# Kernel optimization log

Hardware: AMD Instinct MI355X
Metric: run time of the kernel (lower is better)

## Reference

```python
import jax, jax.numpy as jnp
import numpy as np

N = 100000
E = 1_600_000
IN_CH = 64
HID = 32       # per-head hidden dim
HEADS = 4
OUT_CH = 6
NEG_SLOPE = 0.2


def _glorot(key, shape):
    fan_in, fan_out = shape[0], shape[-1]
    lim = jnp.sqrt(6.0 / (fan_in + fan_out))
    return jax.random.uniform(key, shape, jnp.float32, -lim, lim)


def setup_inputs() -> dict:
    key = jax.random.key(0)
    ks = jax.random.split(key, 20)
    x = jax.random.normal(ks[0], (N, IN_CH), jnp.float32)
    edge_index = jax.random.randint(ks[1], (2, E), 0, N, jnp.int64)
    batch = jnp.zeros((N,), jnp.int64)
    inp = {"x": x, "edge_index": edge_index, "batch": batch}
    inp["W0"] = _glorot(ks[2], (IN_CH, HEADS * HID))
    inp["as0"] = _glorot(ks[3], (HEADS, HID))
    inp["ad0"] = _glorot(ks[4], (HEADS, HID))
    inp["b0"] = jnp.zeros((HEADS * HID,), jnp.float32)
    inp["W1"] = _glorot(ks[5], (HEADS * HID, HEADS * HID))
    inp["as1"] = _glorot(ks[6], (HEADS, HID))
    inp["ad1"] = _glorot(ks[7], (HEADS, HID))
    inp["b1"] = jnp.zeros((HEADS * HID,), jnp.float32)
    inp["W2"] = _glorot(ks[8], (HEADS * HID, HEADS * HID))
    inp["as2"] = _glorot(ks[9], (HEADS, HID))
    inp["ad2"] = _glorot(ks[10], (HEADS, HID))
    inp["b2"] = jnp.zeros((HEADS * HID,), jnp.float32)
    # final layer: 128 -> 6, 1 head, no concat (mean)
    inp["W3"] = _glorot(ks[11], (HEADS * HID, OUT_CH))
    inp["as3"] = _glorot(ks[12], (1, OUT_CH))
    inp["ad3"] = _glorot(ks[13], (1, OUT_CH))
    inp["b3"] = jnp.zeros((OUT_CH,), jnp.float32)
    return inp


def gat_conv(x, src, dst, W, a_src, a_dst, b, heads, concat):
    """PyG GATConv: linear -> per-edge attention -> segment softmax over dst -> scatter-add."""
    n = x.shape[0]
    h = (x @ W).reshape(n, heads, -1)                       # [N,H,D]
    al_s = jnp.sum(h * a_src, axis=-1)                      # [N,H]
    al_d = jnp.sum(h * a_dst, axis=-1)                      # [N,H]
    e = jax.nn.leaky_relu(al_s[src] + al_d[dst], NEG_SLOPE)  # [E,H]
    m = jax.ops.segment_max(e, dst, num_segments=n)         # segment softmax (stable)
    ex = jnp.exp(e - m[dst])
    s = jax.ops.segment_sum(ex, dst, num_segments=n)
    alpha = ex / (s[dst] + 1e-16)                           # [E,H]
    out = jax.ops.segment_sum(alpha[:, :, None] * h[src], dst, num_segments=n)  # [N,H,D]
    out = out.reshape(n, -1) if concat else out.mean(axis=1)
    return out + b


def reference(x, edge_index, batch, W0, as0, ad0, b0, W1, as1, ad1, b1,
              W2, as2, ad2, b2, W3, as3, ad3, b3):
    n = x.shape[0]
    # PyG GATConv adds self-loops by default; edge set is static (no pooling), add once.
    ar = jnp.arange(n, dtype=edge_index.dtype)
    ei = jnp.concatenate([edge_index, jnp.stack([ar, ar])], axis=1)
    src, dst = ei[0], ei[1]
    x = jax.nn.elu(gat_conv(x, src, dst, W0, as0, ad0, b0, HEADS, True))
    x = jax.nn.elu(gat_conv(x, src, dst, W1, as1, ad1, b1, HEADS, True))
    x = jax.nn.elu(gat_conv(x, src, dst, W2, as2, ad2, b2, HEADS, True))
    x = gat_conv(x, src, dst, W3, as3, ad3, b3, 1, False)   # final layer: no activation
    return x
```

## Files before the change

kernel.cpp:

```cpp
#include <hip/hip_runtime.h>
#include <hip/hip_bf16.h>
#include <hip/hip_fp16.h>

#define IN_CH 64
#define HID 32
#define HEADS 4
#define OUT_CH 6
#define NEG_SLOPE 0.2f

typedef __attribute__((ext_vector_type(8))) _Float16 half8;
typedef __attribute__((ext_vector_type(4))) float f32x4;


#define PBLK 256
#define CAP 6144

__global__ __launch_bounds__(256) void part_count(const int* __restrict__ ei, int E, int EN,
                                                  int NB, int epb, int* __restrict__ counts) {
    __shared__ int cnt[512];
    int b = blockIdx.x, t = threadIdx.x;
    for (int i = t; i < NB; i += 256) cnt[i] = 0;
    __syncthreads();
    int e0 = b * epb;
    int e1 = min(e0 + epb, EN);
    for (int e = e0 + t; e < e1; e += 256) {
        int d = (e < E) ? ei[E + e] : (e - E);
        atomicAdd(&cnt[d >> 8], 1);
    }
    __syncthreads();
    for (int i = t; i < NB; i += 256) counts[(size_t)i * PBLK + b] = cnt[i];
}

__global__ __launch_bounds__(256) void bucket_tot(const int* __restrict__ counts,
                                                  int* __restrict__ btot) {
    __shared__ int red[256];
    int k = blockIdx.x, t = threadIdx.x;
    red[t] = counts[(size_t)k * PBLK + t];
    __syncthreads();
    for (int off = 128; off; off >>= 1) {
        if (t < off) red[t] += red[t + off];
        __syncthreads();
    }
    if (t == 0) btot[k] = red[0];
}

__global__ __launch_bounds__(256) void bucket_scan(const int* __restrict__ btot, int NB, int EN,
                                                   int* __restrict__ bstart) {
    __shared__ int tmp[256];
    int t = threadIdx.x;
    int chunk = (NB + 255) >> 8;
    int s0 = t * chunk, s1 = min(s0 + chunk, NB);
    int sum = 0;
    for (int i = s0; i < s1; ++i) sum += btot[i];
    tmp[t] = sum;
    __syncthreads();
    for (int off = 1; off < 256; off <<= 1) {
        int v = (t >= off) ? tmp[t - off] : 0;
        __syncthreads();
        tmp[t] += v;
        __syncthreads();
    }
    int run = (t == 0) ? 0 : tmp[t - 1];
    for (int i = s0; i < s1; ++i) {
        int c = btot[i];
        bstart[i] = run;
        run += c;
    }
    if (t == 255) bstart[NB] = EN;
}

__global__ __launch_bounds__(256) void bucket_base(int* __restrict__ counts,
                                                   const int* __restrict__ bstart) {
    __shared__ int sc[256];
    int k = blockIdx.x, t = threadIdx.x;
    int v = counts[(size_t)k * PBLK + t];
    sc[t] = v;
    __syncthreads();
    for (int off = 1; off < 256; off <<= 1) {
        int u = (t >= off) ? sc[t - off] : 0;
        __syncthreads();
        sc[t] += u;
        __syncthreads();
    }
    counts[(size_t)k * PBLK + t] = bstart[k] + sc[t] - v;
}

__global__ __launch_bounds__(256) void part_scatter(const int* __restrict__ ei, int E, int EN,
                                                    int NB, int epb,
                                                    const int* __restrict__ base,
                                                    int2* __restrict__ ebuf) {
    __shared__ int cur[512];
    int b = blockIdx.x, t = threadIdx.x;
    for (int i = t; i < NB; i += 256) cur[i] = base[(size_t)i * PBLK + b];
    __syncthreads();
    int e0 = b * epb;
    int e1 = min(e0 + epb, EN);
    for (int e = e0 + t; e < e1; e += 256) {
        int s, d;
        if (e < E) { s = ei[e]; d = ei[E + e]; }
        else       { s = e - E; d = s; }
        int slot = atomicAdd(&cur[d >> 8], 1);
        ebuf[slot] = make_int2(s, d & 255);
    }
}

__global__ __launch_bounds__(256) void bucket_csr(const int2* __restrict__ ebuf,
                                                  const int* __restrict__ bstart,
                                                  int NB, int N, int EN,
                                                  int* __restrict__ row_start,
                                                  int* __restrict__ csr_src) {
    __shared__ int cnt[256];
    __shared__ int sc[256];
    __shared__ int stage[CAP];
    int k = blockIdx.x, t = threadIdx.x;
    int s0 = bstart[k], s1 = bstart[k + 1];
    int len = s1 - s0;
    cnt[t] = 0;
    __syncthreads();
    for (int i = t; i < len; i += 256) atomicAdd(&cnt[ebuf[s0 + i].y], 1);
    __syncthreads();
    int v = cnt[t];
    sc[t] = v;
    __syncthreads();
    for (int off = 1; off < 256; off <<= 1) {
        int u = (t >= off) ? sc[t - off] : 0;
        __syncthreads();
        sc[t] += u;
        __syncthreads();
    }
    int excl = sc[t] - v;
    int g = (k << 8) + t;
    if (g < N) row_start[g] = s0 + excl;
    if (k == NB - 1 && t == 0) row_start[N] = EN;
    bool fits = (len <= CAP);
    cnt[t] = fits ? excl : s0 + excl;
    __syncthreads();
    if (fits) {
        for (int i = t; i < len; i += 256) {
            int2 e = ebuf[s0 + i];
            int slot = atomicAdd(&cnt[e.y], 1);
            stage[slot] = e.x;
        }
        __syncthreads();
        for (int i = t; i < len; i += 256) csr_src[s0 + i] = stage[i];
    } else {
        for (int i = t; i < len; i += 256) {
            int2 e = ebuf[s0 + i];
            int slot = atomicAdd(&cnt[e.y], 1);
            csr_src[slot] = e.x;
        }
    }
}


__global__ void wtrans_all(const float* __restrict__ W0, const float* __restrict__ W1,
                           const float* __restrict__ W2, __half* __restrict__ WT0,
                           __half* __restrict__ WT1, __half* __restrict__ WT2) {
    int o = blockIdx.x * blockDim.x + threadIdx.x;
    if (o < 8192) {
        int c = o >> 6, k = o & 63;
        WT0[o] = __float2half(W0[(size_t)k * 128 + c]);
    } else if (o < 8192 + 16384) {
        int i = o - 8192;
        int c = i >> 7, k = i & 127;
        WT1[i] = __float2half(W1[(size_t)k * 128 + c]);
    } else if (o < 8192 + 32768) {
        int i = o - 8192 - 16384;
        int c = i >> 7, k = i & 127;
        WT2[i] = __float2half(W2[(size_t)k * 128 + c]);
    }
}


__global__ __launch_bounds__(256) void gemm_mfma(const __half* __restrict__ A,
                                                 const float* __restrict__ Af,
                                                 const __half* __restrict__ WT,
                                                 const float* __restrict__ avs,
                                                 const float* __restrict__ avd,
                                                 __half* __restrict__ C,
                                                 float* __restrict__ als,
                                                 float* __restrict__ ald,
                                                 int N, int K) {
    int tid = threadIdx.x;
    int wv = tid >> 6, lane = tid & 63;
    int row0 = blockIdx.x * 64 + wv * 16;
    int lrow = lane & 15;
    int lk = (lane >> 4) * 8;
    int garow = row0 + lrow;

    half8 afrag[4];
#pragma unroll
    for (int ks = 0; ks < 4; ++ks) {
        half8 z = {(_Float16)0, (_Float16)0, (_Float16)0, (_Float16)0,
                   (_Float16)0, (_Float16)0, (_Float16)0, (_Float16)0};
        afrag[ks] = z;
    }
    if (garow < N) {
        if (K == 128) {
            const __half* ap = A + (size_t)garow * 128 + lk;
#pragma unroll
            for (int ks = 0; ks < 4; ++ks)
                afrag[ks] = *reinterpret_cast<const half8*>(ap + ks * 32);
        } else {
            const float* ap = Af + (size_t)garow * 64 + lk;
#pragma unroll
            for (int ks = 0; ks < 2; ++ks) {
                float4 f0 = *reinterpret_cast<const float4*>(ap + ks * 32);
                float4 f1 = *reinterpret_cast<const float4*>(ap + ks * 32 + 4);
                half8 fr = {(_Float16)f0.x, (_Float16)f0.y, (_Float16)f0.z, (_Float16)f0.w,
                            (_Float16)f1.x, (_Float16)f1.y, (_Float16)f1.z, (_Float16)f1.w};
                afrag[ks] = fr;
            }
        }
    }

    f32x4 acc[8];
#pragma unroll
    for (int t = 0; t < 8; ++t) acc[t] = (f32x4){0.f, 0.f, 0.f, 0.f};

#pragma unroll
    for (int t = 0; t < 8; ++t) {
        const __half* wb = WT + (size_t)(t * 16 + lrow) * K + lk;
        if (K == 128) {
#pragma unroll
            for (int ks = 0; ks < 4; ++ks) {
                half8 bfrag = *reinterpret_cast<const half8*>(wb + ks * 32);
                acc[t] = __builtin_amdgcn_mfma_f32_16x16x32_f16(afrag[ks], bfrag, acc[t], 0, 0, 0);
            }
        } else {
#pragma unroll
            for (int ks = 0; ks < 2; ++ks) {
                half8 bfrag = *reinterpret_cast<const half8*>(wb + ks * 32);
                acc[t] = __builtin_amdgcn_mfma_f32_16x16x32_f16(afrag[ks], bfrag, acc[t], 0, 0, 0);
            }
        }
    }

    int rbase = (lane >> 4) * 4;
#pragma unroll
    for (int t = 0; t < 8; ++t) {
#pragma unroll
        for (int j = 0; j < 4; ++j) {
            int gr = row0 + rbase + j;
            if (gr < N) C[(size_t)gr * 128 + t * 16 + lrow] = __float2half(acc[t][j]);
        }
    }
    float ps[4][4], pd[4][4];
#pragma unroll
    for (int h = 0; h < 4; ++h)
#pragma unroll
        for (int j = 0; j < 4; ++j) { ps[h][j] = 0.f; pd[h][j] = 0.f; }
#pragma unroll
    for (int t = 0; t < 8; ++t) {
        int ht = t >> 1;
        float as_c = avs[t * 16 + lrow];
        float ad_c = avd[t * 16 + lrow];
#pragma unroll
        for (int j = 0; j < 4; ++j) {
            ps[ht][j] += acc[t][j] * as_c;
            pd[ht][j] += acc[t][j] * ad_c;
        }
    }
#pragma unroll
    for (int h = 0; h < 4; ++h) {
#pragma unroll
        for (int j = 0; j < 4; ++j) {
            float s = ps[h][j], d = pd[h][j];
            s += __shfl_xor(s, 1); d += __shfl_xor(d, 1);
            s += __shfl_xor(s, 2); d += __shfl_xor(d, 2);
            s += __shfl_xor(s, 4); d += __shfl_xor(d, 4);
            s += __shfl_xor(s, 8); d += __shfl_xor(d, 8);
            if (lrow == 0) {
                int gr = row0 + rbase + j;
                if (gr < N) {
                    als[(size_t)gr * 4 + h] = s;
                    ald[(size_t)gr * 4 + h] = d;
                }
            }
        }
    }
}


__device__ __forceinline__ float lrelu(float x) { return x > 0.f ? x : NEG_SLOPE * x; }

__global__ __launch_bounds__(256) void agg_kernel(const __half* __restrict__ h,
                                                  const float* __restrict__ als4,
                                                  const float* __restrict__ ald4,
                                                  const int* __restrict__ row_start,
                                                  const int* __restrict__ csr_src,
                                                  const float* __restrict__ bias,
                                                  __half* __restrict__ xout,
                                                  int N, int applyElu) {
    int v = (int)((blockIdx.x * blockDim.x + threadIdx.x) >> 6);
    int lane = threadIdx.x & 63;
    if (v >= N) return;
    int base = row_start[v], end = row_start[v + 1];

    int half_ = lane >> 5;
    int dim4 = (lane & 31) * 4;
    int hd2  = (lane & 31) >> 3;

    float aldh = ald4[(size_t)v * 4 + hd2];
    float alsh = als4[(size_t)v * 4 + hd2];
    float em = lrelu(alsh + aldh);

    const char* hB = (const char*)h;
    const char* aB = (const char*)als4;
    unsigned dby = (unsigned)dim4 * 2;
    unsigned aby = (unsigned)hd2 * 4;

    float4 acc  = make_float4(0.f, 0.f, 0.f, 0.f);
    float4 acc2 = make_float4(0.f, 0.f, 0.f, 0.f);
    float ssum = 0.f, ssum2 = 0.f;

    union H4 { uint2 u; __half hh[4]; };

    int j = base + half_;
    for (; j + 6 < end; j += 8) {
        unsigned s0 = (unsigned)csr_src[j + 0];
        unsigned s1 = (unsigned)csr_src[j + 2];
        unsigned s2 = (unsigned)csr_src[j + 4];
        unsigned s3 = (unsigned)csr_src[j + 6];
        float a0 = *(const float*)(aB + (s0 << 4) + aby);
        float a1 = *(const float*)(aB + (s1 << 4) + aby);
        float a2 = *(const float*)(aB + (s2 << 4) + aby);
        float a3 = *(const float*)(aB + (s3 << 4) + aby);
        H4 r0, r1, r2, r3;
        r0.u = *(const uint2*)(hB + (s0 << 8) + dby);
        r1.u = *(const uint2*)(hB + (s1 << 8) + dby);
        r2.u = *(const uint2*)(hB + (s2 << 8) + dby);
        r3.u = *(const uint2*)(hB + (s3 << 8) + dby);
        float e0 = __expf(lrelu(a0 + aldh) - em);
        float e1 = __expf(lrelu(a1 + aldh) - em);
        float e2 = __expf(lrelu(a2 + aldh) - em);
        float e3 = __expf(lrelu(a3 + aldh) - em);
        ssum  += e0 + e2;
        ssum2 += e1 + e3;
        acc.x  += e0 * (float)r0.hh[0]; acc.y  += e0 * (float)r0.hh[1];
        acc.z  += e0 * (float)r0.hh[2]; acc.w  += e0 * (float)r0.hh[3];
        acc2.x += e1 * (float)r1.hh[0]; acc2.y += e1 * (float)r1.hh[1];
        acc2.z += e1 * (float)r1.hh[2]; acc2.w += e1 * (float)r1.hh[3];
        acc.x  += e2 * (float)r2.hh[0]; acc.y  += e2 * (float)r2.hh[1];
        acc.z  += e2 * (float)r2.hh[2]; acc.w  += e2 * (float)r2.hh[3];
        acc2.x += e3 * (float)r3.hh[0]; acc2.y += e3 * (float)r3.hh[1];
        acc2.z += e3 * (float)r3.hh[2]; acc2.w += e3 * (float)r3.hh[3];
    }
    for (; j < end; j += 2) {
        unsigned s0 = (unsigned)csr_src[j];
        float a0 = *(const float*)(aB + (s0 << 4) + aby);
        H4 r0;
        r0.u = *(const uint2*)(hB + (s0 << 8) + dby);
        float e0 = __expf(lrelu(a0 + aldh) - em);
        ssum += e0;
        acc.x += e0 * (float)r0.hh[0]; acc.y += e0 * (float)r0.hh[1];
        acc.z += e0 * (float)r0.hh[2]; acc.w += e0 * (float)r0.hh[3];
    }
    acc.x += acc2.x; acc.y += acc2.y; acc.z += acc2.z; acc.w += acc2.w;
    ssum += ssum2;
    acc.x += __shfl_xor(acc.x, 32);
    acc.y += __shfl_xor(acc.y, 32);
    acc.z += __shfl_xor(acc.z, 32);
    acc.w += __shfl_xor(acc.w, 32);
    ssum  += __shfl_xor(ssum, 32);

    if (lane < 32) {
        float inv = 1.0f / (ssum + 1e-16f);
        float4 bv = *reinterpret_cast<const float4*>(bias + dim4);
        float4 o;
        o.x = acc.x * inv + bv.x;
        o.y = acc.y * inv + bv.y;
        o.z = acc.z * inv + bv.z;
        o.w = acc.w * inv + bv.w;
        if (applyElu) {
            o.x = o.x > 0.f ? o.x : expm1f(o.x);
            o.y = o.y > 0.f ? o.y : expm1f(o.y);
            o.z = o.z > 0.f ? o.z : expm1f(o.z);
            o.w = o.w > 0.f ? o.w : expm1f(o.w);
        }
        __half2* op = reinterpret_cast<__half2*>(xout + (size_t)v * 128 + dim4);
        op[0] = __float22half2_rn(make_float2(o.x, o.y));
        op[1] = __float22half2_rn(make_float2(o.z, o.w));
    }
}


__global__ void gemm3_kernel(const __half* __restrict__ x, const float* __restrict__ W,
                             const float* __restrict__ as3, const float* __restrict__ ad3,
                             float* __restrict__ h3p, float* __restrict__ als3,
                             float* __restrict__ ald3, int N) {
    int n = blockIdx.x * blockDim.x + threadIdx.x;
    if (n >= N) return;
    float acc[6] = {0.f, 0.f, 0.f, 0.f, 0.f, 0.f};
    const __half* xp = x + (size_t)n * 128;
#pragma unroll 2
    for (int k8 = 0; k8 < 16; ++k8) {
        union { uint4 u; __half hh[8]; } rv;
        rv.u = *reinterpret_cast<const uint4*>(xp + k8 * 8);
        const float* w0 = W + (size_t)(k8 * 8) * 6;
#pragma unroll
        for (int kk = 0; kk < 8; ++kk) {
            float xv = (float)rv.hh[kk];
#pragma unroll
            for (int q = 0; q < 6; ++q)
                acc[q] += xv * w0[kk * 6 + q];
        }
    }
    float s = 0.f, d = 0.f;
#pragma unroll
    for (int q = 0; q < 6; ++q) {
        s += acc[q] * as3[q];
        d += acc[q] * ad3[q];
    }
    float4* hp = reinterpret_cast<float4*>(h3p + (size_t)n * 8);
    hp[0] = make_float4(acc[0], acc[1], acc[2], acc[3]);
    hp[1] = make_float4(acc[4], acc[5], 0.f, 0.f);
    als3[n] = s;
    ald3[n] = d;
}


__global__ __launch_bounds__(256) void agg3_kernel(const float* __restrict__ h3p,
                                                   const float* __restrict__ als3,
                                                   const float* __restrict__ ald3,
                                                   const int* __restrict__ row_start,
                                                   const int* __restrict__ csr_src,
                                                   const float* __restrict__ b3,
                                                   float* __restrict__ out, int N) {
    int v = (int)((blockIdx.x * blockDim.x + threadIdx.x) >> 5);
    int lane = threadIdx.x & 31;
    if (v >= N) return;
    int base = row_start[v], end = row_start[v + 1];
    int slot = lane >> 3;
    int dim  = lane & 7;

    float aldv = ald3[v];
    float em = lrelu(als3[v] + aldv);
    float acc = 0.f, ssum = 0.f;
    const char* hB = (const char*)h3p;
    const char* aB = (const char*)als3;
    unsigned dby = (unsigned)dim * 4;

    for (int j = base + slot; j < end; j += 4) {
        unsigned s = (unsigned)csr_src[j];
        float a = *(const float*)(aB + (s << 2));
        float hv = *(const float*)(hB + (s << 5) + dby);
        float e = __expf(lrelu(a + aldv) - em);
        ssum += e;
        acc += e * hv;
    }
    acc  += __shfl_xor(acc, 8);
    acc  += __shfl_xor(acc, 16);
    ssum += __shfl_xor(ssum, 8);
    ssum += __shfl_xor(ssum, 16);

    if (slot == 0 && dim < 6) {
        float inv = 1.f / (ssum + 1e-16f);
        out[(size_t)v * 6 + dim] = acc * inv + b3[dim];
    }
}


extern "C" void kernel_launch(void* const* d_in, const int* in_sizes, int n_in,
                              void* d_out, int out_size, void* d_ws, size_t ws_size,
                              hipStream_t stream) {
    const float* x    = (const float*)d_in[0];
    const int*   ei   = (const int*)d_in[1];
    const float* W0   = (const float*)d_in[3];
    const float* as0  = (const float*)d_in[4];
    const float* ad0  = (const float*)d_in[5];
    const float* b0   = (const float*)d_in[6];
    const float* W1   = (const float*)d_in[7];
    const float* as1  = (const float*)d_in[8];
    const float* ad1  = (const float*)d_in[9];
    const float* b1   = (const float*)d_in[10];
    const float* W2   = (const float*)d_in[11];
    const float* as2  = (const float*)d_in[12];
    const float* ad2  = (const float*)d_in[13];
    const float* b2   = (const float*)d_in[14];
    const float* W3   = (const float*)d_in[15];
    const float* as3  = (const float*)d_in[16];
    const float* ad3  = (const float*)d_in[17];
    const float* b3   = (const float*)d_in[18];
    float* out = (float*)d_out;

    int N = in_sizes[0] / IN_CH;
    int E = in_sizes[1] / 2;
    int EN = E + N;
    int NB = (N + 255) >> 8;
    int epb = (EN + PBLK - 1) / PBLK;

    char* p = (char*)d_ws;
    auto alloc = [&](size_t bytes) {
        char* q = p;
        p += (bytes + 255) & ~(size_t)255;
        return q;
    };
    __half* hbuf = (__half*)alloc((size_t)N * 128 * 2);
    __half* xA   = (__half*)alloc((size_t)N * 128 * 2);
    __half* xB   = (__half*)alloc((size_t)N * 128 * 2);
    __half* WT0  = (__half*)alloc((size_t)128 * 64 * 2);
    __half* WT1  = (__half*)alloc((size_t)128 * 128 * 2);
    __half* WT2  = (__half*)alloc((size_t)128 * 128 * 2);
    float* als  = (float*)alloc((size_t)N * 4 * 4);
    float* ald  = (float*)alloc((size_t)N * 4 * 4);
    float* h3p  = (float*)alloc((size_t)N * 8 * 4);
    float* als3 = (float*)alloc((size_t)N * 4);
    float* ald3 = (float*)alloc((size_t)N * 4);
    int* row_start = (int*)alloc((size_t)(N + 1) * 4);
    int* csr_src   = (int*)alloc((size_t)EN * 4);
    int2* ebuf     = (int2*)alloc((size_t)EN * 8);
    int* counts    = (int*)alloc((size_t)NB * PBLK * 4);
    int* btot      = (int*)alloc((size_t)NB * 4);
    int* bstart    = (int*)alloc((size_t)(NB + 1) * 4);
    (void)ws_size; (void)n_in; (void)out_size;

    part_count<<<PBLK, 256, 0, stream>>>(ei, E, EN, NB, epb, counts);
    bucket_tot<<<NB, 256, 0, stream>>>(counts, btot);
    bucket_scan<<<1, 256, 0, stream>>>(btot, NB, EN, bstart);
    bucket_base<<<NB, 256, 0, stream>>>(counts, bstart);
    part_scatter<<<PBLK, 256, 0, stream>>>(ei, E, EN, NB, epb, counts, ebuf);
    bucket_csr<<<NB, 256, 0, stream>>>(ebuf, bstart, NB, N, EN, row_start, csr_src);

    wtrans_all<<<(8192 + 32768 + 255) / 256, 256, 0, stream>>>(W0, W1, W2, WT0, WT1, WT2);

    int gemm_grid = (N + 63) / 64;
    int agg_grid  = (N + 3) / 4;
    int n_grid    = (N + 255) / 256;
    int agg3_grid = (N + 7) / 8;

    gemm_mfma<<<gemm_grid, 256, 0, stream>>>(nullptr, x, WT0, as0, ad0, hbuf, als, ald, N, 64);
    agg_kernel<<<agg_grid, 256, 0, stream>>>(hbuf, als, ald, row_start, csr_src, b0, xA, N, 1);

    gemm_mfma<<<gemm_grid, 256, 0, stream>>>(xA, nullptr, WT1, as1, ad1, hbuf, als, ald, N, 128);
    agg_kernel<<<agg_grid, 256, 0, stream>>>(hbuf, als, ald, row_start, csr_src, b1, xB, N, 1);

    gemm_mfma<<<gemm_grid, 256, 0, stream>>>(xB, nullptr, WT2, as2, ad2, hbuf, als, ald, N, 128);
    agg_kernel<<<agg_grid, 256, 0, stream>>>(hbuf, als, ald, row_start, csr_src, b2, xA, N, 1);

    gemm3_kernel<<<n_grid, 256, 0, stream>>>(xA, W3, as3, ad3, h3p, als3, ald3, N);
    agg3_kernel<<<agg3_grid, 256, 0, stream>>>(h3p, als3, ald3, row_start, csr_src, b3, out, N);
}
```

Before: 443.3 us.

## Fuse edge counting, weight transpose and layer-0 GEMM into one prologue launch

```diff
diff --git a/kernel.cpp b/kernel.cpp
--- a/kernel.cpp
+++ b/kernel.cpp
@@ -11,179 +11,22 @@
 typedef __attribute__((ext_vector_type(8))) _Float16 half8;
 typedef __attribute__((ext_vector_type(4))) float f32x4;
 
-
 #define PBLK 256
 #define CAP 6144
 
-__global__ __launch_bounds__(256) void part_count(const int* __restrict__ ei, int E, int EN,
-                                                  int NB, int epb, int* __restrict__ counts) {
-    __shared__ int cnt[512];
-    int b = blockIdx.x, t = threadIdx.x;
-    for (int i = t; i < NB; i += 256) cnt[i] = 0;
-    __syncthreads();
-    int e0 = b * epb;
-    int e1 = min(e0 + epb, EN);
-    for (int e = e0 + t; e < e1; e += 256) {
-        int d = (e < E) ? ei[E + e] : (e - E);
-        atomicAdd(&cnt[d >> 8], 1);
-    }
-    __syncthreads();
-    for (int i = t; i < NB; i += 256) counts[(size_t)i * PBLK + b] = cnt[i];
-}
-
-__global__ __launch_bounds__(256) void bucket_tot(const int* __restrict__ counts,
-                                                  int* __restrict__ btot) {
-    __shared__ int red[256];
-    int k = blockIdx.x, t = threadIdx.x;
-    red[t] = counts[(size_t)k * PBLK + t];
-    __syncthreads();
-    for (int off = 128; off; off >>= 1) {
-        if (t < off) red[t] += red[t + off];
-        __syncthreads();
-    }
-    if (t == 0) btot[k] = red[0];
-}
-
-__global__ __launch_bounds__(256) void bucket_scan(const int* __restrict__ btot, int NB, int EN,
-                                                   int* __restrict__ bstart) {
-    __shared__ int tmp[256];
-    int t = threadIdx.x;
-    int chunk = (NB + 255) >> 8;
-    int s0 = t * chunk, s1 = min(s0 + chunk, NB);
-    int sum = 0;
-    for (int i = s0; i < s1; ++i) sum += btot[i];
-    tmp[t] = sum;
-    __syncthreads();
-    for (int off = 1; off < 256; off <<= 1) {
-        int v = (t >= off) ? tmp[t - off] : 0;
-        __syncthreads();
-        tmp[t] += v;
-        __syncthreads();
-    }
-    int run = (t == 0) ? 0 : tmp[t - 1];
-    for (int i = s0; i < s1; ++i) {
-        int c = btot[i];
-        bstart[i] = run;
-        run += c;
-    }
-    if (t == 255) bstart[NB] = EN;
-}
-
-__global__ __launch_bounds__(256) void bucket_base(int* __restrict__ counts,
-                                                   const int* __restrict__ bstart) {
-    __shared__ int sc[256];
-    int k = blockIdx.x, t = threadIdx.x;
-    int v = counts[(size_t)k * PBLK + t];
-    sc[t] = v;
-    __syncthreads();
-    for (int off = 1; off < 256; off <<= 1) {
-        int u = (t >= off) ? sc[t - off] : 0;
-        __syncthreads();
-        sc[t] += u;
-        __syncthreads();
-    }
-    counts[(size_t)k * PBLK + t] = bstart[k] + sc[t] - v;
-}
-
-__global__ __launch_bounds__(256) void part_scatter(const int* __restrict__ ei, int E, int EN,
-                                                    int NB, int epb,
-                                                    const int* __restrict__ base,
-                                                    int2* __restrict__ ebuf) {
-    __shared__ int cur[512];
-    int b = blockIdx.x, t = threadIdx.x;
-    for (int i = t; i < NB; i += 256) cur[i] = base[(size_t)i * PBLK + b];
-    __syncthreads();
-    int e0 = b * epb;
-    int e1 = min(e0 + epb, EN);
-    for (int e = e0 + t; e < e1; e += 256) {
-        int s, d;
-        if (e < E) { s = ei[e]; d = ei[E + e]; }
-        else       { s = e - E; d = s; }
-        int slot = atomicAdd(&cur[d >> 8], 1);
-        ebuf[slot] = make_int2(s, d & 255);
-    }
-}
-
-__global__ __launch_bounds__(256) void bucket_csr(const int2* __restrict__ ebuf,
-                                                  const int* __restrict__ bstart,
-                                                  int NB, int N, int EN,
-                                                  int* __restrict__ row_start,
-                                                  int* __restrict__ csr_src) {
-    __shared__ int cnt[256];
-    __shared__ int sc[256];
-    __shared__ int stage[CAP];
-    int k = blockIdx.x, t = threadIdx.x;
-    int s0 = bstart[k], s1 = bstart[k + 1];
-    int len = s1 - s0;
-    cnt[t] = 0;
-    __syncthreads();
-    for (int i = t; i < len; i += 256) atomicAdd(&cnt[ebuf[s0 + i].y], 1);
-    __syncthreads();
-    int v = cnt[t];
-    sc[t] = v;
-    __syncthreads();
-    for (int off = 1; off < 256; off <<= 1) {
-        int u = (t >= off) ? sc[t - off] : 0;
-        __syncthreads();
-        sc[t] += u;
-        __syncthreads();
-    }
-    int excl = sc[t] - v;
-    int g = (k << 8) + t;
-    if (g < N) row_start[g] = s0 + excl;
-    if (k == NB - 1 && t == 0) row_start[N] = EN;
-    bool fits = (len <= CAP);
-    cnt[t] = fits ? excl : s0 + excl;
-    __syncthreads();
-    if (fits) {
-        for (int i = t; i < len; i += 256) {
-            int2 e = ebuf[s0 + i];
-            int slot = atomicAdd(&cnt[e.y], 1);
-            stage[slot] = e.x;
-        }
-        __syncthreads();
-        for (int i = t; i < len; i += 256) csr_src[s0 + i] = stage[i];
-    } else {
-        for (int i = t; i < len; i += 256) {
-            int2 e = ebuf[s0 + i];
-            int slot = atomicAdd(&cnt[e.y], 1);
-            csr_src[slot] = e.x;
-        }
-    }
-}
-
-
-__global__ void wtrans_all(const float* __restrict__ W0, const float* __restrict__ W1,
-                           const float* __restrict__ W2, __half* __restrict__ WT0,
-                           __half* __restrict__ WT1, __half* __restrict__ WT2) {
-    int o = blockIdx.x * blockDim.x + threadIdx.x;
-    if (o < 8192) {
-        int c = o >> 6, k = o & 63;
-        WT0[o] = __float2half(W0[(size_t)k * 128 + c]);
-    } else if (o < 8192 + 16384) {
-        int i = o - 8192;
-        int c = i >> 7, k = i & 127;
-        WT1[i] = __float2half(W1[(size_t)k * 128 + c]);
-    } else if (o < 8192 + 32768) {
-        int i = o - 8192 - 16384;
-        int c = i >> 7, k = i & 127;
-        WT2[i] = __float2half(W2[(size_t)k * 128 + c]);
-    }
-}
-
-
-__global__ __launch_bounds__(256) void gemm_mfma(const __half* __restrict__ A,
-                                                 const float* __restrict__ Af,
-                                                 const __half* __restrict__ WT,
-                                                 const float* __restrict__ avs,
-                                                 const float* __restrict__ avd,
-                                                 __half* __restrict__ C,
-                                                 float* __restrict__ als,
-                                                 float* __restrict__ ald,
-                                                 int N, int K) {
-    int tid = threadIdx.x;
+
+__device__ __forceinline__ void gemm_tile(const __half* __restrict__ A,
+                                          const float* __restrict__ Af,
+                                          const __half* __restrict__ WT,
+                                          const float* __restrict__ Wf,
+                                          const float* __restrict__ avs,
+                                          const float* __restrict__ avd,
+                                          __half* __restrict__ C,
+                                          float* __restrict__ als,
+                                          float* __restrict__ ald,
+                                          int N, int K, int blk, int tid) {
     int wv = tid >> 6, lane = tid & 63;
-    int row0 = blockIdx.x * 64 + wv * 16;
+    int row0 = blk * 64 + wv * 16;
     int lrow = lane & 15;
     int lk = (lane >> 4) * 8;
     int garow = row0 + lrow;
@@ -220,17 +63,22 @@
 
 #pragma unroll
     for (int t = 0; t < 8; ++t) {
-        const __half* wb = WT + (size_t)(t * 16 + lrow) * K + lk;
+        int c = t * 16 + lrow;
         if (K == 128) {
+            const __half* wb = WT + (size_t)c * 128 + lk;
 #pragma unroll
             for (int ks = 0; ks < 4; ++ks) {
                 half8 bfrag = *reinterpret_cast<const half8*>(wb + ks * 32);
                 acc[t] = __builtin_amdgcn_mfma_f32_16x16x32_f16(afrag[ks], bfrag, acc[t], 0, 0, 0);
             }
         } else {
+            const float* wcol = Wf + c;
 #pragma unroll
             for (int ks = 0; ks < 2; ++ks) {
-                half8 bfrag = *reinterpret_cast<const half8*>(wb + ks * 32);
+                half8 bfrag;
+#pragma unroll
+                for (int jj = 0; jj < 8; ++jj)
+                    bfrag[jj] = (_Float16)wcol[(size_t)(ks * 32 + lk + jj) * 128];
                 acc[t] = __builtin_amdgcn_mfma_f32_16x16x32_f16(afrag[ks], bfrag, acc[t], 0, 0, 0);
             }
         }
@@ -277,6 +125,179 @@
                     ald[(size_t)gr * 4 + h] = d;
                 }
             }
+        }
+    }
+}
+
+
+__global__ __launch_bounds__(256) void prologue_kernel(
+        const int* __restrict__ ei, int E, int EN, int NB, int epb,
+        int* __restrict__ counts,
+        const float* __restrict__ W1, const float* __restrict__ W2,
+        __half* __restrict__ WT1, __half* __restrict__ WT2,
+        const float* __restrict__ x, const float* __restrict__ W0,
+        const float* __restrict__ avs, const float* __restrict__ avd,
+        __half* __restrict__ C, float* __restrict__ als, float* __restrict__ ald,
+        int N) {
+    __shared__ int cnt[512];
+    int b = blockIdx.x, t = threadIdx.x;
+    if (b < PBLK) {
+        for (int i = t; i < NB; i += 256) cnt[i] = 0;
+        __syncthreads();
+        int e0 = b * epb;
+        int e1 = min(e0 + epb, EN);
+        for (int e = e0 + t; e < e1; e += 256) {
+            int d = (e < E) ? ei[E + e] : (e - E);
+            atomicAdd(&cnt[d >> 8], 1);
+        }
+        __syncthreads();
+        for (int i = t; i < NB; i += 256) counts[(size_t)i * PBLK + b] = cnt[i];
+    } else if (b < PBLK + 128) {
+        int i = (b - PBLK) * 256 + t;
+        if (i < 16384) {
+            int c = i >> 7, k = i & 127;
+            WT1[i] = __float2half(W1[(size_t)k * 128 + c]);
+        } else {
+            int i2 = i - 16384;
+            int c = i2 >> 7, k = i2 & 127;
+            WT2[i2] = __float2half(W2[(size_t)k * 128 + c]);
+        }
+    } else {
+        gemm_tile(nullptr, x, nullptr, W0, avs, avd, C, als, ald, N, 64, b - PBLK - 128, t);
+    }
+}
+
+
+__global__ __launch_bounds__(256) void gemm_mfma(const __half* __restrict__ A,
+                                                 const __half* __restrict__ WT,
+                                                 const float* __restrict__ avs,
+                                                 const float* __restrict__ avd,
+                                                 __half* __restrict__ C,
+                                                 float* __restrict__ als,
+                                                 float* __restrict__ ald,
+                                                 int N) {
+    gemm_tile(A, nullptr, WT, nullptr, avs, avd, C, als, ald, N, 128,
+              blockIdx.x, threadIdx.x);
+}
+
+
+__global__ __launch_bounds__(256) void bucket_tot(const int* __restrict__ counts,
+                                                  int* __restrict__ btot) {
+    __shared__ int red[256];
+    int k = blockIdx.x, t = threadIdx.x;
+    red[t] = counts[(size_t)k * PBLK + t];
+    __syncthreads();
+    for (int off = 128; off; off >>= 1) {
+        if (t < off) red[t] += red[t + off];
+        __syncthreads();
+    }
+    if (t == 0) btot[k] = red[0];
+}
+
+__global__ __launch_bounds__(256) void bucket_scan(const int* __restrict__ btot, int NB, int EN,
+                                                   int* __restrict__ bstart) {
+    __shared__ int tmp[256];
+    int t = threadIdx.x;
+    int chunk = (NB + 255) >> 8;
+    int s0 = t * chunk, s1 = min(s0 + chunk, NB);
+    int sum = 0;
+    for (int i = s0; i < s1; ++i) sum += btot[i];
+    tmp[t] = sum;
+    __syncthreads();
+    for (int off = 1; off < 256; off <<= 1) {
+        int v = (t >= off) ? tmp[t - off] : 0;
+        __syncthreads();
+        tmp[t] += v;
+        __syncthreads();
+    }
+    int run = (t == 0) ? 0 : tmp[t - 1];
+    for (int i = s0; i < s1; ++i) {
+        int c = btot[i];
+        bstart[i] = run;
+        run += c;
+    }
+    if (t == 255) bstart[NB] = EN;
+}
+
+__global__ __launch_bounds__(256) void bucket_base(int* __restrict__ counts,
+                                                   const int* __restrict__ bstart) {
+    __shared__ int sc[256];
+    int k = blockIdx.x, t = threadIdx.x;
+    int v = counts[(size_t)k * PBLK + t];
+    sc[t] = v;
+    __syncthreads();
+    for (int off = 1; off < 256; off <<= 1) {
+        int u = (t >= off) ? sc[t - off] : 0;
+        __syncthreads();
+        sc[t] += u;
+        __syncthreads();
+    }
+    counts[(size_t)k * PBLK + t] = bstart[k] + sc[t] - v;
+}
+
+__global__ __launch_bounds__(256) void part_scatter(const int* __restrict__ ei, int E, int EN,
+                                                    int NB, int epb,
+                                                    const int* __restrict__ base,
+                                                    int* __restrict__ ebuf) {
+    __shared__ int cur[512];
+    int b = blockIdx.x, t = threadIdx.x;
+    for (int i = t; i < NB; i += 256) cur[i] = base[(size_t)i * PBLK + b];
+    __syncthreads();
+    int e0 = b * epb;
+    int e1 = min(e0 + epb, EN);
+    for (int e = e0 + t; e < e1; e += 256) {
+        int s, d;
+        if (e < E) { s = ei[e]; d = ei[E + e]; }
+        else       { s = e - E; d = s; }
+        int slot = atomicAdd(&cur[d >> 8], 1);
+        ebuf[slot] = (s << 8) | (d & 255);
+    }
+}
+
+__global__ __launch_bounds__(256) void bucket_csr(const int* __restrict__ ebuf,
+                                                  const int* __restrict__ bstart,
+                                                  int NB, int N, int EN,
+                                                  int* __restrict__ row_start,
+                                                  int* __restrict__ csr_src) {
+    __shared__ int cnt[256];
+    __shared__ int sc[256];
+    __shared__ int stage[CAP];
+    int k = blockIdx.x, t = threadIdx.x;
+    int s0 = bstart[k], s1 = bstart[k + 1];
+    int len = s1 - s0;
+    cnt[t] = 0;
+    __syncthreads();
+    for (int i = t; i < len; i += 256) atomicAdd(&cnt[ebuf[s0 + i] & 255], 1);
+    __syncthreads();
+    int v = cnt[t];
+    sc[t] = v;
+    __syncthreads();
+    for (int off = 1; off < 256; off <<= 1) {
+        int u = (t >= off) ? sc[t - off] : 0;
+        __syncthreads();
+        sc[t] += u;
+        __syncthreads();
+    }
+    int excl = sc[t] - v;
+    int g = (k << 8) + t;
+    if (g < N) row_start[g] = s0 + excl;
+    if (k == NB - 1 && t == 0) row_start[N] = EN;
+    bool fits = (len <= CAP);
+    cnt[t] = fits ? excl : s0 + excl;
+    __syncthreads();
+    if (fits) {
+        for (int i = t; i < len; i += 256) {
+            int e = ebuf[s0 + i];
+            int slot = atomicAdd(&cnt[e & 255], 1);
+            stage[slot] = (int)((unsigned)e >> 8);
+        }
+        __syncthreads();
+        for (int i = t; i < len; i += 256) csr_src[s0 + i] = stage[i];
+    } else {
+        for (int i = t; i < len; i += 256) {
+            int e = ebuf[s0 + i];
+            int slot = atomicAdd(&cnt[e & 255], 1);
+            csr_src[slot] = (int)((unsigned)e >> 8);
         }
     }
 }
@@ -499,7 +520,6 @@
     __half* hbuf = (__half*)alloc((size_t)N * 128 * 2);
     __half* xA   = (__half*)alloc((size_t)N * 128 * 2);
     __half* xB   = (__half*)alloc((size_t)N * 128 * 2);
-    __half* WT0  = (__half*)alloc((size_t)128 * 64 * 2);
     __half* WT1  = (__half*)alloc((size_t)128 * 128 * 2);
     __half* WT2  = (__half*)alloc((size_t)128 * 128 * 2);
     float* als  = (float*)alloc((size_t)N * 4 * 4);
@@ -509,33 +529,33 @@
     float* ald3 = (float*)alloc((size_t)N * 4);
     int* row_start = (int*)alloc((size_t)(N + 1) * 4);
     int* csr_src   = (int*)alloc((size_t)EN * 4);
-    int2* ebuf     = (int2*)alloc((size_t)EN * 8);
+    int* ebuf      = (int*)alloc((size_t)EN * 4);
     int* counts    = (int*)alloc((size_t)NB * PBLK * 4);
     int* btot      = (int*)alloc((size_t)NB * 4);
     int* bstart    = (int*)alloc((size_t)(NB + 1) * 4);
     (void)ws_size; (void)n_in; (void)out_size;
 
-    part_count<<<PBLK, 256, 0, stream>>>(ei, E, EN, NB, epb, counts);
+    int gemm_grid = (N + 63) / 64;
+    int agg_grid  = (N + 3) / 4;
+    int n_grid    = (N + 255) / 256;
+    int agg3_grid = (N + 7) / 8;
+
+    prologue_kernel<<<PBLK + 128 + gemm_grid, 256, 0, stream>>>(
+        ei, E, EN, NB, epb, counts, W1, W2, WT1, WT2,
+        x, W0, as0, ad0, hbuf, als, ald, N);
+
     bucket_tot<<<NB, 256, 0, stream>>>(counts, btot);
     bucket_scan<<<1, 256, 0, stream>>>(btot, NB, EN, bstart);
     bucket_base<<<NB, 256, 0, stream>>>(counts, bstart);
     part_scatter<<<PBLK, 256, 0, stream>>>(ei, E, EN, NB, epb, counts, ebuf);
     bucket_csr<<<NB, 256, 0, stream>>>(ebuf, bstart, NB, N, EN, row_start, csr_src);
 
-    wtrans_all<<<(8192 + 32768 + 255) / 256, 256, 0, stream>>>(W0, W1, W2, WT0, WT1, WT2);
-
-    int gemm_grid = (N + 63) / 64;
-    int agg_grid  = (N + 3) / 4;
-    int n_grid    = (N + 255) / 256;
-    int agg3_grid = (N + 7) / 8;
-
-    gemm_mfma<<<gemm_grid, 256, 0, stream>>>(nullptr, x, WT0, as0, ad0, hbuf, als, ald, N, 64);
     agg_kernel<<<agg_grid, 256, 0, stream>>>(hbuf, als, ald, row_start, csr_src, b0, xA, N, 1);
 
-    gemm_mfma<<<gemm_grid, 256, 0, stream>>>(xA, nullptr, WT1, as1, ad1, hbuf, als, ald, N, 128);
+    gemm_mfma<<<gemm_grid, 256, 0, stream>>>(xA, WT1, as1, ad1, hbuf, als, ald, N);
     agg_kernel<<<agg_grid, 256, 0, stream>>>(hbuf, als, ald, row_start, csr_src, b1, xB, N, 1);
 
-    gemm_mfma<<<gemm_grid, 256, 0, stream>>>(xB, nullptr, WT2, as2, ad2, hbuf, als, ald, N, 128);
+    gemm_mfma<<<gemm_grid, 256, 0, stream>>>(xB, WT2, as2, ad2, hbuf, als, ald, N);
     agg_kernel<<<agg_grid, 256, 0, stream>>>(hbuf, als, ald, row_start, csr_src, b2, xA, N, 1);
 
     gemm3_kernel<<<n_grid, 256, 0, stream>>>(xA, W3, as3, ad3, h3p, als3, ald3, N);
```

New measurement: 421.5 us, median of 2. 4.9% less time.
